# Optimization experiments

Hardware: AMD Instinct MI355X
Metric: run time of the kernel (lower is better)

Reference implementation:

```python
import jax, jax.numpy as jnp
import numpy as np

N_QUBITS = 12
N_LAYERS = 4
DIM = 2 ** N_QUBITS  # 4096
BATCH = 128
NUM_CLASSES = 10


def _rot_matrix(phi, theta, omega):
    # PennyLane Rot(phi, theta, omega) = RZ(omega) @ RY(theta) @ RZ(phi)
    c = jnp.cos(theta * 0.5)
    s = jnp.sin(theta * 0.5)
    ep = jnp.exp(-0.5j * (phi + omega))  # e^{-i(phi+omega)/2}
    em = jnp.exp(0.5j * (phi - omega))   # e^{ i(phi-omega)/2}
    row0 = jnp.stack([ep * c, -em * s])
    row1 = jnp.stack([jnp.conj(em) * s, jnp.conj(ep) * c])
    return jnp.stack([row0, row1]).astype(jnp.complex64)  # (2,2)


def _apply_single(psi, u, q):
    # psi: (B, 2^n); wire 0 is the most-significant bit (PennyLane convention)
    b = psi.shape[0]
    s = psi.reshape(b, 2 ** q, 2, -1)
    s = jnp.einsum('ab,kxbz->kxaz', u, s)
    return s.reshape(b, -1)


def _apply_cnot(psi, c, t, n):
    b = psi.shape[0]
    s = psi.reshape((b,) + (2,) * n)
    ac, at = c + 1, t + 1  # +1 for batch axis
    s0 = jax.lax.index_in_dim(s, 0, ac, keepdims=True)
    s1 = jax.lax.index_in_dim(s, 1, ac, keepdims=True)
    s1 = jnp.flip(s1, axis=at)  # X on target where control == 1
    s = jnp.concatenate([s0, s1], axis=ac)
    return s.reshape(b, -1)


def _pauliz_signs(n):
    idx = np.arange(2 ** n)
    bits = (idx[None, :] >> (n - 1 - np.arange(n)[:, None])) & 1  # wire 0 = MSB
    return jnp.asarray(1.0 - 2.0 * bits, dtype=jnp.float32)  # (n, 2^n)


def setup_inputs() -> dict:
    key = jax.random.key(0)
    k = jax.random.split(key, 6)
    inputs = jax.random.normal(k[0], (BATCH, DIM), dtype=jnp.float32)
    W_pre = jax.random.normal(k[1], (DIM, DIM), dtype=jnp.float32) / np.sqrt(DIM)
    b_pre = jax.random.normal(k[2], (DIM,), dtype=jnp.float32) * 0.01
    q_weights = jax.random.uniform(k[3], (N_LAYERS, N_QUBITS, 3), dtype=jnp.float32,
                                   minval=0.0, maxval=2.0 * np.pi)
    W_fc = jax.random.normal(k[4], (NUM_CLASSES, N_QUBITS), dtype=jnp.float32) / np.sqrt(N_QUBITS)
    b_fc = jax.random.normal(k[5], (NUM_CLASSES,), dtype=jnp.float32) * 0.01
    return {"inputs": inputs, "W_pre": W_pre, "b_pre": b_pre,
            "q_weights": q_weights, "W_fc": W_fc, "b_fc": b_fc}


def reference(inputs, W_pre, b_pre, q_weights, W_fc, b_fc):
    n = N_QUBITS
    # pre_pqc Linear + exact GELU (torch default)
    x = inputs @ W_pre.T + b_pre
    x = jax.nn.gelu(x, approximate=False)
    # AmplitudeEmbedding(normalize=True)
    norm = jnp.sqrt(jnp.sum(x * x, axis=1, keepdims=True))
    psi = (x / norm).astype(jnp.complex64)  # (B, 2^n)
    # N_LAYERS repetitions of StronglyEntanglingLayers (each has N_LAYERS layers)
    for _rep in range(N_LAYERS):
        for l in range(N_LAYERS):
            for q in range(n):
                u = _rot_matrix(q_weights[l, q, 0], q_weights[l, q, 1], q_weights[l, q, 2])
                psi = _apply_single(psi, u, q)
            r = l % (n - 1) + 1  # default ranges of StronglyEntanglingLayers
            for q in range(n):
                psi = _apply_cnot(psi, q, (q + r) % n, n)
    probs = psi.real ** 2 + psi.imag ** 2  # (B, 2^n)
    z = probs @ _pauliz_signs(n).T  # (B, n): <Z_i>
    return z @ W_fc.T + b_fc
```

## Files before the change

kernel.cpp:

```cpp
#include <hip/hip_runtime.h>
#include <math.h>

#define DIM 4096
#define NQ 12
#define BATCH 128
#define BN 32
#define BK 64
#define ZSTR (128 * DIM)

typedef __attribute__((ext_vector_type(8))) short bf16x8;
typedef __attribute__((ext_vector_type(4))) float f32x4;
typedef unsigned int uint2v __attribute__((ext_vector_type(2)));

__device__ __forceinline__ unsigned short f2bf(float f) {
    union { float f; unsigned int u; } c; c.f = f;
    unsigned int u = c.u;
    unsigned int r = u + 0x7fffu + ((u >> 16) & 1u);
    return (unsigned short)(r >> 16);
}

__global__ __launch_bounds__(256) void gemm_bf16_kernel(
    const float* __restrict__ A, const float* __restrict__ W,
    float* __restrict__ psum, int splitk)
{
    __shared__ unsigned short As[128][BK + 8];
    __shared__ unsigned short Bs[BN][BK + 8];

    const int t  = threadIdx.x;
    const int bn = blockIdx.x * BN;
    const int z  = blockIdx.y;
    const int krange = DIM / splitk;
    const int kstart = z * krange;
    const int kend = kstart + krange;
    const int w = t >> 6;
    const int l = t & 63;
    const int m0w = w * 32;

    f32x4 acc[2][2] = {};
    float4 pa[8], pb[2];

    auto load_tiles = [&](int k0) {
#pragma unroll
        for (int i = 0; i < 8; ++i) {
            const int fid = t + i * 256;
            pa[i] = *(const float4*)(A + (size_t)(fid >> 4) * DIM + k0 + (fid & 15) * 4);
        }
#pragma unroll
        for (int i = 0; i < 2; ++i) {
            const int fid = t + i * 256;
            pb[i] = *(const float4*)(W + (size_t)(bn + (fid >> 4)) * DIM + k0 + (fid & 15) * 4);
        }
    };

    load_tiles(kstart);
    for (int k0 = kstart; k0 < kend; k0 += BK) {
        __syncthreads();
#pragma unroll
        for (int i = 0; i < 8; ++i) {
            const int fid = t + i * 256;
            const int row = fid >> 4, c4 = (fid & 15) * 4;
            union { unsigned short h[4]; uint2 u; } pk;
            pk.h[0] = f2bf(pa[i].x); pk.h[1] = f2bf(pa[i].y);
            pk.h[2] = f2bf(pa[i].z); pk.h[3] = f2bf(pa[i].w);
            *(uint2*)&As[row][c4] = pk.u;
        }
#pragma unroll
        for (int i = 0; i < 2; ++i) {
            const int fid = t + i * 256;
            const int row = fid >> 4, c4 = (fid & 15) * 4;
            union { unsigned short h[4]; uint2 u; } pk;
            pk.h[0] = f2bf(pb[i].x); pk.h[1] = f2bf(pb[i].y);
            pk.h[2] = f2bf(pb[i].z); pk.h[3] = f2bf(pb[i].w);
            *(uint2*)&Bs[row][c4] = pk.u;
        }
        const int kn = (k0 + BK < kend) ? (k0 + BK) : k0;
        load_tiles(kn);
        __syncthreads();
#pragma unroll
        for (int kk = 0; kk < 2; ++kk) {
            const int kc = kk * 32 + (l >> 4) * 8;
            bf16x8 a0 = *(const bf16x8*)&As[m0w +      (l & 15)][kc];
            bf16x8 a1 = *(const bf16x8*)&As[m0w + 16 + (l & 15)][kc];
            bf16x8 b0 = *(const bf16x8*)&Bs[      (l & 15)][kc];
            bf16x8 b1 = *(const bf16x8*)&Bs[16 + (l & 15)][kc];
            acc[0][0] = __builtin_amdgcn_mfma_f32_16x16x32_bf16(a0, b0, acc[0][0], 0, 0, 0);
            acc[0][1] = __builtin_amdgcn_mfma_f32_16x16x32_bf16(a0, b1, acc[0][1], 0, 0, 0);
            acc[1][0] = __builtin_amdgcn_mfma_f32_16x16x32_bf16(a1, b0, acc[1][0], 0, 0, 0);
            acc[1][1] = __builtin_amdgcn_mfma_f32_16x16x32_bf16(a1, b1, acc[1][1], 0, 0, 0);
        }
    }
#pragma unroll
    for (int mf = 0; mf < 2; ++mf)
#pragma unroll
        for (int nf = 0; nf < 2; ++nf)
#pragma unroll
            for (int r = 0; r < 4; ++r) {
                const int m = m0w + mf * 16 + (l >> 4) * 4 + r;
                const int n = bn + nf * 16 + (l & 15);
                psum[(size_t)z * ZSTR + (size_t)m * DIM + n] = acc[mf][nf][r];
            }
}

template<int CTRL>
__device__ __forceinline__ float fdpp(float v) {
    return __int_as_float(__builtin_amdgcn_update_dpp(
        0, __float_as_int(v), CTRL, 0xF, 0xF, false));
}
__device__ __forceinline__ float pl16_partner(float v) {
#if __has_builtin(__builtin_amdgcn_permlane16_swap)
    uint2v r = __builtin_amdgcn_permlane16_swap(__float_as_uint(v), __float_as_uint(v), false, false);
    return __uint_as_float(r.x ^ r.y ^ __float_as_uint(v));
#else
    float a = v, b = v;
    asm volatile("v_permlane16_swap_b32 %0, %1" : "+v"(a), "+v"(b));
    return __uint_as_float(__float_as_uint(a) ^ __float_as_uint(b) ^ __float_as_uint(v));
#endif
}
__device__ __forceinline__ float pl32_partner(float v) {
#if __has_builtin(__builtin_amdgcn_permlane32_swap)
    uint2v r = __builtin_amdgcn_permlane32_swap(__float_as_uint(v), __float_as_uint(v), false, false);
    return __uint_as_float(r.x ^ r.y ^ __float_as_uint(v));
#else
    float a = v, b = v;
    asm volatile("v_permlane32_swap_b32 %0, %1" : "+v"(a), "+v"(b));
    return __uint_as_float(__float_as_uint(a) ^ __float_as_uint(b) ^ __float_as_uint(v));
#endif
}

__global__ __launch_bounds__(1024) void circuit_kernel(
    const float* __restrict__ psum, int splitk, const float* __restrict__ bias,
    const float* __restrict__ qw, const float* __restrict__ Wfc,
    const float* __restrict__ bfc, float* __restrict__ out)
{
    __shared__ float2 sbuf[2][4096];
    __shared__ float4 gm4[48][2];
    __shared__ int   sspj[4][4];
    __shared__ float redw[16];
    __shared__ float zred[16][12];
    __shared__ float zbit[12];

    const int t = threadIdx.x;
    const int b = blockIdx.x;
    const int wv = t >> 6;
    const int l6 = t & 63;
    const int w01 = wv & 3;
    const int w23 = wv >> 2;

    if (t < 48) {
        const int base = t * 3;
        const float phi = qw[base + 0], th = qw[base + 1], om = qw[base + 2];
        float c, s, chp, shp, chm, shm;
        sincosf(0.5f * th, &s, &c);
        sincosf(0.5f * (phi + om), &shp, &chp);
        sincosf(0.5f * (phi - om), &shm, &chm);
        float* g = (float*)&gm4[t][0];
        g[0] =  c * chp;  g[1] = -c * shp;
        g[2] = -s * chm;  g[3] = -s * shm;
        g[4] =  s * chm;  g[5] = -s * shm;
        g[6] =  c * chp;  g[7] =  c * shp;
    }
#define SWZ(x) ((x) ^ (((x) >> 4) & 15))
#define SIG3(x) (((((x) >> 8) & 3) << 10) | (((x) & 3) << 8) | ((((x) >> 2) & 63) << 2) | (((x) >> 10) & 3))
    if (t < 16) {
        const int ll = t >> 2, r = ll + 1;
        int u = t & 3;
        for (int q = 11; q >= 0; --q) {
            const int bc = 11 - q, bt2 = 11 - ((q + r) % 12);
            u ^= ((u >> bc) & 1) << bt2;
        }
        int s3 = SIG3(u);
        sspj[ll][t & 3] = SWZ(s3);
    }
    int ssfb[4];
#pragma unroll
    for (int ll = 0; ll < 4; ++ll) {
        const int r = ll + 1;
        int u = t << 2;
        for (int q = 11; q >= 0; --q) {
            const int bc = 11 - q, bt2 = 11 - ((q + r) % 12);
            u ^= ((u >> bc) & 1) << bt2;
        }
        int s3 = SIG3(u);
        ssfb[ll] = SWZ(s3);
    }
    const int b1w = SWZ((w23 << 8) | (l6 << 2) | w01);
    const int b1r = SWZ((w01 << 10) | (w23 << 8) | (l6 << 2));
    const int b2w = SWZ((w01 << 8) | (l6 << 2) | w23);
    const int b2r = SWZ((w23 << 10) | (w01 << 8) | (l6 << 2));

    float a0 = 0.f, a1 = 0.f, a2 = 0.f, a3 = 0.f;
    for (int z = 0; z < splitk; ++z) {
        const float4 p = *(const float4*)(psum + (size_t)z * ZSTR + (size_t)b * DIM + t * 4);
        a0 += p.x; a1 += p.y; a2 += p.z; a3 += p.w;
    }
    {
        const float4 bb = *(const float4*)(bias + t * 4);
        a0 += bb.x; a1 += bb.y; a2 += bb.z; a3 += bb.w;
    }
    float xr[4];
    xr[0] = 0.5f * a0 * (1.0f + erff(a0 * 0.70710678118654752f));
    xr[1] = 0.5f * a1 * (1.0f + erff(a1 * 0.70710678118654752f));
    xr[2] = 0.5f * a2 * (1.0f + erff(a2 * 0.70710678118654752f));
    xr[3] = 0.5f * a3 * (1.0f + erff(a3 * 0.70710678118654752f));
    float ss = xr[0]*xr[0] + xr[1]*xr[1] + xr[2]*xr[2] + xr[3]*xr[3];
#pragma unroll
    for (int off = 32; off; off >>= 1) ss += __shfl_xor(ss, off);
    if (l6 == 0) redw[wv] = ss;
    __syncthreads();
    float tot = 0.f;
#pragma unroll
    for (int i = 0; i < 16; ++i) tot += redw[i];
    const float rn = 1.0f / sqrtf(tot);

    float sr[4], si[4];
#pragma unroll
    for (int j = 0; j < 4; ++j) { sr[j] = xr[j] * rn; si[j] = 0.f; }

    auto reg_gate = [&](int lb, float4 g0, float4 g1) {
#pragma unroll
        for (int p = 0; p < 2; ++p) {
            const int j0 = (lb == 0) ? (p << 1) : p;
            const int j1 = j0 | (1 << lb);
            const float ar = sr[j0], ai = si[j0];
            const float br = sr[j1], bi = si[j1];
            sr[j0] = g0.x * ar - g0.y * ai + g0.z * br - g0.w * bi;
            si[j0] = g0.x * ai + g0.y * ar + g0.z * bi + g0.w * br;
            sr[j1] = g1.x * ar - g1.y * ai + g1.z * br - g1.w * bi;
            si[j1] = g1.x * ai + g1.y * ar + g1.z * bi + g1.w * br;
        }
    };
    auto lane_gate = [&](int lanebit, auto&& partner, float4 g0, float4 g1) {
        const int bsel = (l6 >> lanebit) & 1;
        const float cAr = bsel ? g1.z : g0.x, cAi = bsel ? g1.w : g0.y;
        const float cBr = bsel ? g1.x : g0.z, cBi = bsel ? g1.y : g0.w;
#pragma unroll
        for (int j = 0; j < 4; ++j) {
            const float pr = partner(sr[j]), pi = partner(si[j]);
            const float nr = cAr * sr[j] - cAi * si[j] + cBr * pr - cBi * pi;
            const float ni = cAr * si[j] + cAi * sr[j] + cBr * pi + cBi * pr;
            sr[j] = nr; si[j] = ni;
        }
    };

    int tb = 0;
    for (int rep = 0; rep < 4; ++rep) {
#pragma unroll
        for (int l = 0; l < 4; ++l) {
            const int gb = l * 12;
            reg_gate(0, gm4[gb + 11][0], gm4[gb + 11][1]);
            reg_gate(1, gm4[gb + 10][0], gm4[gb + 10][1]);
            lane_gate(0, [](float v) { return fdpp<0xB1>(v); },               gm4[gb + 9][0], gm4[gb + 9][1]);
            lane_gate(1, [](float v) { return fdpp<0x4E>(v); },               gm4[gb + 8][0], gm4[gb + 8][1]);
            lane_gate(2, [](float v) { return fdpp<0x1B>(fdpp<0x141>(v)); },  gm4[gb + 7][0], gm4[gb + 7][1]);
            lane_gate(3, [](float v) { return fdpp<0x141>(fdpp<0x140>(v)); }, gm4[gb + 6][0], gm4[gb + 6][1]);
            lane_gate(4, [](float v) { return pl16_partner(v); },             gm4[gb + 5][0], gm4[gb + 5][1]);
            lane_gate(5, [](float v) { return pl32_partner(v); },             gm4[gb + 4][0], gm4[gb + 4][1]);
#pragma unroll
            for (int j = 0; j < 4; ++j) sbuf[tb][b1w ^ (j << 10)] = make_float2(sr[j], si[j]);
            __syncthreads();
#pragma unroll
            for (int j = 0; j < 4; ++j) { float2 a = sbuf[tb][b1r ^ j]; sr[j] = a.x; si[j] = a.y; }
            tb ^= 1;
            reg_gate(0, gm4[gb + 3][0], gm4[gb + 3][1]);
            reg_gate(1, gm4[gb + 2][0], gm4[gb + 2][1]);
#pragma unroll
            for (int j = 0; j < 4; ++j) sbuf[tb][b2w ^ (j << 10)] = make_float2(sr[j], si[j]);
            __syncthreads();
#pragma unroll
            for (int j = 0; j < 4; ++j) { float2 a = sbuf[tb][b2r ^ j]; sr[j] = a.x; si[j] = a.y; }
            tb ^= 1;
            reg_gate(0, gm4[gb + 1][0], gm4[gb + 1][1]);
            reg_gate(1, gm4[gb + 0][0], gm4[gb + 0][1]);
#pragma unroll
            for (int j = 0; j < 4; ++j) sbuf[tb][b2r ^ j] = make_float2(sr[j], si[j]);
            __syncthreads();
#pragma unroll
            for (int j = 0; j < 4; ++j) { float2 a = sbuf[tb][ssfb[l] ^ sspj[l][j]]; sr[j] = a.x; si[j] = a.y; }
            tb ^= 1;
        }
    }

    float p0 = sr[0]*sr[0] + si[0]*si[0];
    float p1 = sr[1]*sr[1] + si[1]*si[1];
    float p2 = sr[2]*sr[2] + si[2]*si[2];
    float p3 = sr[3]*sr[3] + si[3]*si[3];
    const float psumv = p0 + p1 + p2 + p3;
    float zp[12];
    zp[0] = p0 - p1 + p2 - p3;
    zp[1] = p0 + p1 - p2 - p3;
#pragma unroll
    for (int bp = 2; bp < 12; ++bp)
        zp[bp] = ((t >> (bp - 2)) & 1) ? -psumv : psumv;
#pragma unroll
    for (int bp = 0; bp < 12; ++bp) {
        float vv = zp[bp];
#pragma unroll
        for (int off = 32; off; off >>= 1) vv += __shfl_xor(vv, off);
        if (l6 == 0) zred[wv][bp] = vv;
    }
    __syncthreads();
    if (t < 12) {
        float vv = 0.f;
#pragma unroll
        for (int w2 = 0; w2 < 16; ++w2) vv += zred[w2][t];
        zbit[t] = vv;
    }
    __syncthreads();
    if (t < 10) {
        float o = bfc[t];
#pragma unroll
        for (int q = 0; q < NQ; ++q) o = fmaf(zbit[11 - q], Wfc[t * NQ + q], o);
        out[b * 10 + t] = o;
    }
#undef SWZ
#undef SIG3
}

extern "C" void kernel_launch(void* const* d_in, const int* in_sizes, int n_in,
                              void* d_out, int out_size, void* d_ws, size_t ws_size,
                              hipStream_t stream)
{
    const float* inputs = (const float*)d_in[0];
    const float* W_pre  = (const float*)d_in[1];
    const float* b_pre  = (const float*)d_in[2];
    const float* q_w    = (const float*)d_in[3];
    const float* W_fc   = (const float*)d_in[4];
    const float* b_fc   = (const float*)d_in[5];
    float* outp = (float*)d_out;
    float* psum = (float*)d_ws;

    const size_t slab = (size_t)ZSTR * sizeof(float);
    int splitk = 4;
    if (ws_size < 4 * slab) splitk = 2;
    if (ws_size < 2 * slab) splitk = 1;

    dim3 g1(DIM / BN, splitk);
    gemm_bf16_kernel<<<g1, 256, 0, stream>>>(inputs, W_pre, psum, splitk);
    circuit_kernel<<<BATCH, 1024, 0, stream>>>(psum, splitk, b_pre, q_w, W_fc, b_fc, outp);
}
```

Measured before the change: 98.29 us.

## Cut circuit shared-memory exchanges from three to two per layer and pack complex math

Changes the per-layer qubit-to-thread mapping so that after the first LDS transpose, two more qubits sit on DPP lanes. The layer then needs only two shared-memory exchanges and barriers instead of three. Complex amplitudes are held as two-float vectors with a swap-negate trick, which may let the compiler emit packed FP32 math. The swizzle and permutation index calculations are reworked to match, so a mistake there would silently corrupt the state mapping.

```diff
diff --git a/kernel.cpp b/kernel.cpp
--- a/kernel.cpp
+++ b/kernel.cpp
@@ -10,6 +10,7 @@
 
 typedef __attribute__((ext_vector_type(8))) short bf16x8;
 typedef __attribute__((ext_vector_type(4))) float f32x4;
+typedef __attribute__((ext_vector_type(2))) float f32x2;
 typedef unsigned int uint2v __attribute__((ext_vector_type(2)));
 
 __device__ __forceinline__ unsigned short f2bf(float f) {
@@ -132,7 +133,7 @@
     const float* __restrict__ qw, const float* __restrict__ Wfc,
     const float* __restrict__ bfc, float* __restrict__ out)
 {
-    __shared__ float2 sbuf[2][4096];
+    __shared__ f32x2 sbuf[2][4096];
     __shared__ float4 gm4[48][2];
     __shared__ int   sspj[4][4];
     __shared__ float redw[16];
@@ -159,8 +160,7 @@
         g[4] =  s * chm;  g[5] = -s * shm;
         g[6] =  c * chp;  g[7] =  c * shp;
     }
-#define SWZ(x) ((x) ^ (((x) >> 4) & 15))
-#define SIG3(x) (((((x) >> 8) & 3) << 10) | (((x) & 3) << 8) | ((((x) >> 2) & 63) << 2) | (((x) >> 10) & 3))
+#define SWZ2(x) ((x) ^ (((x) >> 4) & 15) ^ (((x) >> 10) & 3))
     if (t < 16) {
         const int ll = t >> 2, r = ll + 1;
         int u = t & 3;
@@ -168,8 +168,7 @@
             const int bc = 11 - q, bt2 = 11 - ((q + r) % 12);
             u ^= ((u >> bc) & 1) << bt2;
         }
-        int s3 = SIG3(u);
-        sspj[ll][t & 3] = SWZ(s3);
+        sspj[ll][t & 3] = SWZ2(u);
     }
     int ssfb[4];
 #pragma unroll
@@ -180,13 +179,12 @@
             const int bc = 11 - q, bt2 = 11 - ((q + r) % 12);
             u ^= ((u >> bc) & 1) << bt2;
         }
-        int s3 = SIG3(u);
-        ssfb[ll] = SWZ(s3);
-    }
-    const int b1w = SWZ((w23 << 8) | (l6 << 2) | w01);
-    const int b1r = SWZ((w01 << 10) | (w23 << 8) | (l6 << 2));
-    const int b2w = SWZ((w01 << 8) | (l6 << 2) | w23);
-    const int b2r = SWZ((w23 << 10) | (w01 << 8) | (l6 << 2));
+        ssfb[ll] = SWZ2(u);
+    }
+    const int s0base = (w23 << 10) | (w01 << 8) | (l6 << 2);
+    const int base0  = SWZ2(s0base);
+    const int s1base = ((l6 & 3) << 10) | ((l6 >> 2) << 4) | (w23 << 2) | w01;
+    const int base1  = SWZ2(s1base);
 
     float a0 = 0.f, a1 = 0.f, a2 = 0.f, a3 = 0.f;
     for (int z = 0; z < splitk; ++z) {
@@ -212,21 +210,20 @@
     for (int i = 0; i < 16; ++i) tot += redw[i];
     const float rn = 1.0f / sqrtf(tot);
 
-    float sr[4], si[4];
-#pragma unroll
-    for (int j = 0; j < 4; ++j) { sr[j] = xr[j] * rn; si[j] = 0.f; }
-
+    f32x2 s[4];
+#pragma unroll
+    for (int j = 0; j < 4; ++j) s[j] = (f32x2){xr[j] * rn, 0.f};
+
+    auto swapneg = [](f32x2 v) { return (f32x2){-v.y, v.x}; };
     auto reg_gate = [&](int lb, float4 g0, float4 g1) {
 #pragma unroll
         for (int p = 0; p < 2; ++p) {
             const int j0 = (lb == 0) ? (p << 1) : p;
             const int j1 = j0 | (1 << lb);
-            const float ar = sr[j0], ai = si[j0];
-            const float br = sr[j1], bi = si[j1];
-            sr[j0] = g0.x * ar - g0.y * ai + g0.z * br - g0.w * bi;
-            si[j0] = g0.x * ai + g0.y * ar + g0.z * bi + g0.w * br;
-            sr[j1] = g1.x * ar - g1.y * ai + g1.z * br - g1.w * bi;
-            si[j1] = g1.x * ai + g1.y * ar + g1.z * bi + g1.w * br;
+            const f32x2 a = s[j0], bb2 = s[j1];
+            const f32x2 aw = swapneg(a), bw = swapneg(bb2);
+            s[j0] = g0.x * a + g0.y * aw + g0.z * bb2 + g0.w * bw;
+            s[j1] = g1.x * a + g1.y * aw + g1.z * bb2 + g1.w * bw;
         }
     };
     auto lane_gate = [&](int lanebit, auto&& partner, float4 g0, float4 g1) {
@@ -235,10 +232,9 @@
         const float cBr = bsel ? g1.x : g0.z, cBi = bsel ? g1.y : g0.w;
 #pragma unroll
         for (int j = 0; j < 4; ++j) {
-            const float pr = partner(sr[j]), pi = partner(si[j]);
-            const float nr = cAr * sr[j] - cAi * si[j] + cBr * pr - cBi * pi;
-            const float ni = cAr * si[j] + cAi * sr[j] + cBr * pi + cBi * pr;
-            sr[j] = nr; si[j] = ni;
+            const f32x2 p = (f32x2){partner(s[j].x), partner(s[j].y)};
+            const f32x2 pw = swapneg(p), sw = swapneg(s[j]);
+            s[j] = cAr * s[j] + cAi * sw + cBr * p + cBi * pw;
         }
     };
 
@@ -247,43 +243,37 @@
 #pragma unroll
         for (int l = 0; l < 4; ++l) {
             const int gb = l * 12;
-            reg_gate(0, gm4[gb + 11][0], gm4[gb + 11][1]);
-            reg_gate(1, gm4[gb + 10][0], gm4[gb + 10][1]);
             lane_gate(0, [](float v) { return fdpp<0xB1>(v); },               gm4[gb + 9][0], gm4[gb + 9][1]);
             lane_gate(1, [](float v) { return fdpp<0x4E>(v); },               gm4[gb + 8][0], gm4[gb + 8][1]);
             lane_gate(2, [](float v) { return fdpp<0x1B>(fdpp<0x141>(v)); },  gm4[gb + 7][0], gm4[gb + 7][1]);
             lane_gate(3, [](float v) { return fdpp<0x141>(fdpp<0x140>(v)); }, gm4[gb + 6][0], gm4[gb + 6][1]);
             lane_gate(4, [](float v) { return pl16_partner(v); },             gm4[gb + 5][0], gm4[gb + 5][1]);
             lane_gate(5, [](float v) { return pl32_partner(v); },             gm4[gb + 4][0], gm4[gb + 4][1]);
-#pragma unroll
-            for (int j = 0; j < 4; ++j) sbuf[tb][b1w ^ (j << 10)] = make_float2(sr[j], si[j]);
+            reg_gate(0, gm4[gb + 11][0], gm4[gb + 11][1]);
+            reg_gate(1, gm4[gb + 10][0], gm4[gb + 10][1]);
+#pragma unroll
+            for (int j = 0; j < 4; ++j) sbuf[tb][base0 ^ j] = s[j];
             __syncthreads();
 #pragma unroll
-            for (int j = 0; j < 4; ++j) { float2 a = sbuf[tb][b1r ^ j]; sr[j] = a.x; si[j] = a.y; }
+            for (int j = 0; j < 4; ++j) s[j] = sbuf[tb][base1 ^ (j << 8)];
             tb ^= 1;
+            lane_gate(0, [](float v) { return fdpp<0xB1>(v); }, gm4[gb + 1][0], gm4[gb + 1][1]);
+            lane_gate(1, [](float v) { return fdpp<0x4E>(v); }, gm4[gb + 0][0], gm4[gb + 0][1]);
             reg_gate(0, gm4[gb + 3][0], gm4[gb + 3][1]);
             reg_gate(1, gm4[gb + 2][0], gm4[gb + 2][1]);
 #pragma unroll
-            for (int j = 0; j < 4; ++j) sbuf[tb][b2w ^ (j << 10)] = make_float2(sr[j], si[j]);
+            for (int j = 0; j < 4; ++j) sbuf[tb][base1 ^ (j << 8)] = s[j];
             __syncthreads();
 #pragma unroll
-            for (int j = 0; j < 4; ++j) { float2 a = sbuf[tb][b2r ^ j]; sr[j] = a.x; si[j] = a.y; }
+            for (int j = 0; j < 4; ++j) s[j] = sbuf[tb][ssfb[l] ^ sspj[l][j]];
             tb ^= 1;
-            reg_gate(0, gm4[gb + 1][0], gm4[gb + 1][1]);
-            reg_gate(1, gm4[gb + 0][0], gm4[gb + 0][1]);
-#pragma unroll
-            for (int j = 0; j < 4; ++j) sbuf[tb][b2r ^ j] = make_float2(sr[j], si[j]);
-            __syncthreads();
-#pragma unroll
-            for (int j = 0; j < 4; ++j) { float2 a = sbuf[tb][ssfb[l] ^ sspj[l][j]]; sr[j] = a.x; si[j] = a.y; }
-            tb ^= 1;
-        }
-    }
-
-    float p0 = sr[0]*sr[0] + si[0]*si[0];
-    float p1 = sr[1]*sr[1] + si[1]*si[1];
-    float p2 = sr[2]*sr[2] + si[2]*si[2];
-    float p3 = sr[3]*sr[3] + si[3]*si[3];
+        }
+    }
+
+    const float p0 = s[0].x * s[0].x + s[0].y * s[0].y;
+    const float p1 = s[1].x * s[1].x + s[1].y * s[1].y;
+    const float p2 = s[2].x * s[2].x + s[2].y * s[2].y;
+    const float p3 = s[3].x * s[3].x + s[3].y * s[3].y;
     const float psumv = p0 + p1 + p2 + p3;
     float zp[12];
     zp[0] = p0 - p1 + p2 - p3;
@@ -312,8 +302,7 @@
         for (int q = 0; q < NQ; ++q) o = fmaf(zbit[11 - q], Wfc[t * NQ + q], o);
         out[b * 10 + t] = o;
     }
-#undef SWZ
-#undef SIG3
+#undef SWZ2
 }
 
 extern "C" void kernel_launch(void* const* d_in, const int* in_sizes, int n_in,
```

Result: slower. 109.5 us (+11.4%).

## Cut circuit layer transposes from three LDS round-trips to two with lane gates

Applied to the files above, without the earlier changes.

The circuit kernel now handles each entangling layer with two shared-memory exchanges instead of three. After the first transpose, two qubits that previously needed a third transpose are applied as DPP lane gates. Gate coefficients are pre-arranged per lane-bit selection (gsel/grow1) so lane gates load a single float4 without per-element selects. The CNOT permutation offsets are held in registers instead of shared memory, and new swizzle formulas are used. Launch bounds add a minimum-blocks hint, which adds register pressure and makes correctness depend on the new index mappings.

```diff
diff --git a/kernel.cpp b/kernel.cpp
--- a/kernel.cpp
+++ b/kernel.cpp
@@ -127,14 +127,17 @@
 #endif
 }
 
-__global__ __launch_bounds__(1024) void circuit_kernel(
+#define SWZ2(x) ((x) ^ (((x) >> 4) & 15) ^ (((x) >> 10) & 3))
+#define FB(x)   ((x) ^ (((x) >> 4) & 15) ^ (((x) >> 10) & 3) ^ ((((x) ^ ((x) >> 8)) & 3) << 2))
+
+__global__ __launch_bounds__(1024, 4) void circuit_kernel(
     const float* __restrict__ psum, int splitk, const float* __restrict__ bias,
     const float* __restrict__ qw, const float* __restrict__ Wfc,
     const float* __restrict__ bfc, float* __restrict__ out)
 {
     __shared__ float2 sbuf[2][4096];
-    __shared__ float4 gm4[48][2];
-    __shared__ int   sspj[4][4];
+    __shared__ float4 gsel[48][2];
+    __shared__ float4 grow1[48];
     __shared__ float redw[16];
     __shared__ float zred[16][12];
     __shared__ float zbit[12];
@@ -153,25 +156,16 @@
         sincosf(0.5f * th, &s, &c);
         sincosf(0.5f * (phi + om), &shp, &chp);
         sincosf(0.5f * (phi - om), &shm, &chm);
-        float* g = (float*)&gm4[t][0];
-        g[0] =  c * chp;  g[1] = -c * shp;
-        g[2] = -s * chm;  g[3] = -s * shm;
-        g[4] =  s * chm;  g[5] = -s * shm;
-        g[6] =  c * chp;  g[7] =  c * shp;
-    }
-#define SWZ(x) ((x) ^ (((x) >> 4) & 15))
-#define SIG3(x) (((((x) >> 8) & 3) << 10) | (((x) & 3) << 8) | ((((x) >> 2) & 63) << 2) | (((x) >> 10) & 3))
-    if (t < 16) {
-        const int ll = t >> 2, r = ll + 1;
-        int u = t & 3;
-        for (int q = 11; q >= 0; --q) {
-            const int bc = 11 - q, bt2 = 11 - ((q + r) % 12);
-            u ^= ((u >> bc) & 1) << bt2;
-        }
-        int s3 = SIG3(u);
-        sspj[ll][t & 3] = SWZ(s3);
-    }
-    int ssfb[4];
+        const float u00r =  c * chp, u00i = -c * shp;
+        const float u01r = -s * chm, u01i = -s * shm;
+        const float u10r =  s * chm, u10i = -s * shm;
+        const float u11r =  c * chp, u11i =  c * shp;
+        gsel[t][0] = make_float4(u00r, u00i, u01r, u01i);
+        gsel[t][1] = make_float4(u11r, u11i, u10r, u10i);
+        grow1[t]   = make_float4(u10r, u10i, u11r, u11i);
+    }
+
+    int ssfb[4], sspjv[4][4];
 #pragma unroll
     for (int ll = 0; ll < 4; ++ll) {
         const int r = ll + 1;
@@ -180,13 +174,27 @@
             const int bc = 11 - q, bt2 = 11 - ((q + r) % 12);
             u ^= ((u >> bc) & 1) << bt2;
         }
-        int s3 = SIG3(u);
-        ssfb[ll] = SWZ(s3);
-    }
-    const int b1w = SWZ((w23 << 8) | (l6 << 2) | w01);
-    const int b1r = SWZ((w01 << 10) | (w23 << 8) | (l6 << 2));
-    const int b2w = SWZ((w01 << 8) | (l6 << 2) | w23);
-    const int b2r = SWZ((w23 << 10) | (w01 << 8) | (l6 << 2));
+        ssfb[ll] = FB(u);
+        sspjv[ll][0] = 0;
+#pragma unroll
+        for (int j = 1; j < 4; ++j) {
+            int v = j;
+            for (int q = 11; q >= 0; --q) {
+                const int bc = 11 - q, bt2 = 11 - ((q + r) % 12);
+                v ^= ((v >> bc) & 1) << bt2;
+            }
+            sspjv[ll][j] = FB(v);
+        }
+    }
+
+    const int s0base = (w23 << 10) | (w01 << 8) | (l6 << 2);
+    const int base0  = SWZ2(s0base);
+    const int s1base = ((l6 & 3) << 10) | ((l6 >> 2) << 4) | (w23 << 2) | w01;
+    const int base1  = SWZ2(s1base);
+    const int fb1    = FB(s1base);
+
+    const int bs0 = l6 & 1, bs1 = (l6 >> 1) & 1, bs2 = (l6 >> 2) & 1;
+    const int bs3 = (l6 >> 3) & 1, bs4 = (l6 >> 4) & 1, bs5 = (l6 >> 5) & 1;
 
     float a0 = 0.f, a1 = 0.f, a2 = 0.f, a3 = 0.f;
     for (int z = 0; z < splitk; ++z) {
@@ -229,61 +237,65 @@
             si[j1] = g1.x * ai + g1.y * ar + g1.z * bi + g1.w * br;
         }
     };
-    auto lane_gate = [&](int lanebit, auto&& partner, float4 g0, float4 g1) {
-        const int bsel = (l6 >> lanebit) & 1;
-        const float cAr = bsel ? g1.z : g0.x, cAi = bsel ? g1.w : g0.y;
-        const float cBr = bsel ? g1.x : g0.z, cBi = bsel ? g1.y : g0.w;
+    auto lane_gate = [&](auto&& partner, float4 gs) {
 #pragma unroll
         for (int j = 0; j < 4; ++j) {
             const float pr = partner(sr[j]), pi = partner(si[j]);
-            const float nr = cAr * sr[j] - cAi * si[j] + cBr * pr - cBi * pi;
-            const float ni = cAr * si[j] + cAi * sr[j] + cBr * pi + cBi * pr;
+            const float nr = gs.x * sr[j] - gs.y * si[j] + gs.z * pr - gs.w * pi;
+            const float ni = gs.x * si[j] + gs.y * sr[j] + gs.z * pi + gs.w * pr;
             sr[j] = nr; si[j] = ni;
         }
     };
 
-    int tb = 0;
     for (int rep = 0; rep < 4; ++rep) {
 #pragma unroll
         for (int l = 0; l < 4; ++l) {
             const int gb = l * 12;
-            reg_gate(0, gm4[gb + 11][0], gm4[gb + 11][1]);
-            reg_gate(1, gm4[gb + 10][0], gm4[gb + 10][1]);
-            lane_gate(0, [](float v) { return fdpp<0xB1>(v); },               gm4[gb + 9][0], gm4[gb + 9][1]);
-            lane_gate(1, [](float v) { return fdpp<0x4E>(v); },               gm4[gb + 8][0], gm4[gb + 8][1]);
-            lane_gate(2, [](float v) { return fdpp<0x1B>(fdpp<0x141>(v)); },  gm4[gb + 7][0], gm4[gb + 7][1]);
-            lane_gate(3, [](float v) { return fdpp<0x141>(fdpp<0x140>(v)); }, gm4[gb + 6][0], gm4[gb + 6][1]);
-            lane_gate(4, [](float v) { return pl16_partner(v); },             gm4[gb + 5][0], gm4[gb + 5][1]);
-            lane_gate(5, [](float v) { return pl32_partner(v); },             gm4[gb + 4][0], gm4[gb + 4][1]);
-#pragma unroll
-            for (int j = 0; j < 4; ++j) sbuf[tb][b1w ^ (j << 10)] = make_float2(sr[j], si[j]);
+            const float4 gA2 = gsel[gb + 9][bs0], gA3 = gsel[gb + 8][bs1];
+            const float4 gA4 = gsel[gb + 7][bs2], gA5 = gsel[gb + 6][bs3];
+            const float4 gA6 = gsel[gb + 5][bs4], gA7 = gsel[gb + 4][bs5];
+            const float4 rAa0 = gsel[gb + 11][0], rAb0 = grow1[gb + 11];
+            const float4 rAa1 = gsel[gb + 10][0], rAb1 = grow1[gb + 10];
+            lane_gate([](float v) { return fdpp<0xB1>(v); },               gA2);
+            lane_gate([](float v) { return fdpp<0x4E>(v); },               gA3);
+            lane_gate([](float v) { return fdpp<0x1B>(fdpp<0x141>(v)); },  gA4);
+            lane_gate([](float v) { return fdpp<0x141>(fdpp<0x140>(v)); }, gA5);
+            lane_gate([](float v) { return pl16_partner(v); },             gA6);
+            lane_gate([](float v) { return pl32_partner(v); },             gA7);
+            reg_gate(0, rAa0, rAb0);
+            reg_gate(1, rAa1, rAb1);
+#pragma unroll
+            for (int j = 0; j < 4; ++j)
+                sbuf[0][base0 ^ j] = make_float2(sr[j], si[j]);
             __syncthreads();
 #pragma unroll
-            for (int j = 0; j < 4; ++j) { float2 a = sbuf[tb][b1r ^ j]; sr[j] = a.x; si[j] = a.y; }
-            tb ^= 1;
-            reg_gate(0, gm4[gb + 3][0], gm4[gb + 3][1]);
-            reg_gate(1, gm4[gb + 2][0], gm4[gb + 2][1]);
-#pragma unroll
-            for (int j = 0; j < 4; ++j) sbuf[tb][b2w ^ (j << 10)] = make_float2(sr[j], si[j]);
+            for (int j = 0; j < 4; ++j) {
+                float2 a = sbuf[0][base1 ^ (j << 8)];
+                sr[j] = a.x; si[j] = a.y;
+            }
+            const float4 gB0 = gsel[gb + 1][bs0], gB1 = gsel[gb + 0][bs1];
+            const float4 rBa0 = gsel[gb + 3][0], rBb0 = grow1[gb + 3];
+            const float4 rBa1 = gsel[gb + 2][0], rBb1 = grow1[gb + 2];
+            lane_gate([](float v) { return fdpp<0xB1>(v); }, gB0);
+            lane_gate([](float v) { return fdpp<0x4E>(v); }, gB1);
+            reg_gate(0, rBa0, rBb0);
+            reg_gate(1, rBa1, rBb1);
+#pragma unroll
+            for (int j = 0; j < 4; ++j)
+                sbuf[1][fb1 ^ (j << 8) ^ (j << 2)] = make_float2(sr[j], si[j]);
             __syncthreads();
 #pragma unroll
-            for (int j = 0; j < 4; ++j) { float2 a = sbuf[tb][b2r ^ j]; sr[j] = a.x; si[j] = a.y; }
-            tb ^= 1;
-            reg_gate(0, gm4[gb + 1][0], gm4[gb + 1][1]);
-            reg_gate(1, gm4[gb + 0][0], gm4[gb + 0][1]);
-#pragma unroll
-            for (int j = 0; j < 4; ++j) sbuf[tb][b2r ^ j] = make_float2(sr[j], si[j]);
-            __syncthreads();
-#pragma unroll
-            for (int j = 0; j < 4; ++j) { float2 a = sbuf[tb][ssfb[l] ^ sspj[l][j]]; sr[j] = a.x; si[j] = a.y; }
-            tb ^= 1;
-        }
-    }
-
-    float p0 = sr[0]*sr[0] + si[0]*si[0];
-    float p1 = sr[1]*sr[1] + si[1]*si[1];
-    float p2 = sr[2]*sr[2] + si[2]*si[2];
-    float p3 = sr[3]*sr[3] + si[3]*si[3];
+            for (int j = 0; j < 4; ++j) {
+                float2 a = sbuf[1][ssfb[l] ^ sspjv[l][j]];
+                sr[j] = a.x; si[j] = a.y;
+            }
+        }
+    }
+
+    const float p0 = sr[0]*sr[0] + si[0]*si[0];
+    const float p1 = sr[1]*sr[1] + si[1]*si[1];
+    const float p2 = sr[2]*sr[2] + si[2]*si[2];
+    const float p3 = sr[3]*sr[3] + si[3]*si[3];
     const float psumv = p0 + p1 + p2 + p3;
     float zp[12];
     zp[0] = p0 - p1 + p2 - p3;
@@ -312,8 +324,6 @@
         for (int q = 0; q < NQ; ++q) o = fmaf(zbit[11 - q], Wfc[t * NQ + q], o);
         out[b * 10 + t] = o;
     }
-#undef SWZ
-#undef SIG3
 }
 
 extern "C" void kernel_launch(void* const* d_in, const int* in_sizes, int n_in,
```

Result: slower. 103.6 us (+5.4%).
